# Performance work log

Measured on AMD Instinct MI355X. Metric: run time of the kernel, lower is better.

Reference implementation:

```python
import jax, jax.numpy as jnp
import numpy as np

GRID = (32, 32)          # 448 // 14
IMG = (448, 448)
SIGMA = 4.0              # anomalib AnomalyMapGenerator default smoothing


def _l2norm(x, axis=-1, eps=1e-12):
    return x / jnp.clip(jnp.linalg.norm(x, axis=axis, keepdims=True), eps, None)


def _gaussian_blur(x, sigma=SIGMA):
    # kornia-style: kernel_size = 2*int(4*sigma+0.5)+1, reflect padding, separable conv
    radius = int(4.0 * sigma + 0.5)
    t = jnp.arange(-radius, radius + 1, dtype=x.dtype)
    k = jnp.exp(-0.5 * (t / sigma) ** 2)
    k = k / k.sum()
    xp = jnp.pad(x, ((0, 0), (0, 0), (radius, radius), (radius, radius)), mode='reflect')
    kh = k.reshape(1, 1, -1, 1)
    kw = k.reshape(1, 1, 1, -1)
    dn = ('NCHW', 'OIHW', 'NCHW')
    y = jax.lax.conv_general_dilated(xp, kh, (1, 1), 'VALID', dimension_numbers=dn)
    return jax.lax.conv_general_dilated(y, kw, (1, 1), 'VALID', dimension_numbers=dn)


def setup_inputs() -> dict:
    key = jax.random.key(0)
    k1, k2 = jax.random.split(key)
    features = jax.random.normal(k1, (8, 1024, 384), dtype=jnp.float32)
    memory_bank = jax.random.normal(k2, (65536, 384), dtype=jnp.float32)
    return {"features": features, "memory_bank": memory_bank}


def reference(features, memory_bank):
    # features: (B, N, D) patch tokens from DINOv2; memory_bank: (M, D)
    b, n, _ = features.shape
    f = _l2norm(features)                 # F.normalize(features, p=2, dim=1) on flattened patches
    mb = _l2norm(memory_bank)             # bank stores normalized embeddings
    sim = jnp.einsum('bnd,md->bnm', f, mb)            # (B, N, M) cosine similarity
    dists = jnp.clip(1.0 - sim, 0.0, 2.0)
    min_dists = dists.min(axis=2)                     # k = num_neighbours = 1 -> row min
    num_top = max(int(n * 0.01), 1)
    top_vals = jax.lax.top_k(min_dists, num_top)[0]
    pred_score = top_vals.mean(axis=1, keepdims=True) # (B, 1)
    amap = min_dists.reshape(b, 1, *GRID)
    amap = jax.image.resize(amap, (b, 1, *IMG), method='bilinear')
    anomaly_map = _gaussian_blur(amap)                # (B, 1, H, W)
    return pred_score, anomaly_map
```

## Files before the change

kernel.cpp:

```cpp
#include <hip/hip_runtime.h>
#include <hip/hip_bf16.h>

#define NROW_F 8192
#define NROW_B 65536
#define KDIM   384
#define BM 128
#define BN 128
#define NSUB 16
#define NGRP (NROW_B / (BN * NSUB))
#define NBM  (NROW_F / BM)
#define NWG  (NBM * NGRP)

#define LDSA 0
#define LDSS2 0
#define LDSR2 16384
#define LDSB 49152
#define LDS_TOT 81920

typedef int   i32x4 __attribute__((ext_vector_type(4)));
typedef float f32x4 __attribute__((ext_vector_type(4)));

static __device__ __forceinline__ void stage16(const void* g, void* l) {
  __builtin_amdgcn_global_load_lds(
      (const __attribute__((address_space(1))) unsigned int*)g,
      (__attribute__((address_space(3))) unsigned int*)l, 16, 0, 0);
}

__global__ __launch_bounds__(256) void quantize_rows_kernel(
    const float* __restrict__ in, char* __restrict__ out8,
    float* __restrict__ scales, int nrows) {
  int row = blockIdx.x * 8 + (threadIdx.x >> 5);
  int l   = threadIdx.x & 31;
  if (row >= nrows) return;
  const f32x4* r = (const f32x4*)(in + (size_t)row * KDIM);
  f32x4 v[3];
  float ss = 0.f, mx = 0.f;
#pragma unroll
  for (int i = 0; i < 3; ++i) {
    v[i] = r[l + i * 32];
#pragma unroll
    for (int j = 0; j < 4; ++j) {
      ss += v[i][j] * v[i][j];
      mx = fmaxf(mx, fabsf(v[i][j]));
    }
  }
#pragma unroll
  for (int d = 1; d < 32; d <<= 1) {
    ss += __shfl_xor(ss, d, 64);
    mx = fmaxf(mx, __shfl_xor(mx, d, 64));
  }
  mx = fmaxf(mx, 1e-30f);
  float inv = rsqrtf(fmaxf(ss, 1e-24f));
  float scl = 127.0f / mx;
  if (l == 0) scales[row] = mx * inv * (1.0f / 127.0f);
  char* o = out8 + (size_t)row * KDIM;
#pragma unroll
  for (int i = 0; i < 3; ++i) {
    char4 c;
    c.x = (char)__float2int_rn(v[i][0] * scl);
    c.y = (char)__float2int_rn(v[i][1] * scl);
    c.z = (char)__float2int_rn(v[i][2] * scl);
    c.w = (char)__float2int_rn(v[i][3] * scl);
    *(char4*)(o + (l + i * 32) * 4) = c;
  }
}

__global__ __launch_bounds__(256, 2) void maxsim_kernel(
    const char* __restrict__ F8,
    const char* __restrict__ B8,
    const float* __restrict__ sA,
    const float* __restrict__ sB,
    float* __restrict__ partial) {
  __shared__ __align__(16) char smem[LDS_TOT];

  const int tid  = threadIdx.x;
  const int wv   = tid >> 6;
  const int lane = tid & 63;
  const int l15  = lane & 15;
  const int lhi  = lane >> 4;
  const int wr   = wv >> 1;
  const int wc   = wv & 1;

  const int wg  = (blockIdx.x & 7) * (NWG / 8) + (blockIdx.x >> 3);
  const int bm  = wg & (NBM - 1);
  const int grp = wg >> 6;
  const size_t brow = (size_t)bm * BM;

  const int srow = tid >> 2;
  const int gsw  = (tid & 3) ^ ((tid >> 3) & 3);

  {
    const char* gA = F8 + (size_t)(brow + srow) * KDIM + gsw * 16;
    char* lA = smem + LDSA + wv * 1024;
#pragma unroll
    for (int kt = 0; kt < 6; ++kt) {
      stage16(gA + kt * 64,             lA + kt * 8192);
      stage16(gA + kt * 64 + 64 * KDIM, lA + kt * 8192 + 4096);
    }
  }
  asm volatile("s_waitcnt vmcnt(0)" ::: "memory");
  __builtin_amdgcn_s_barrier();

  const int cof = ((l15 >> 1) & 3) << 4;
  auto ldA8 = [&](int k6, int m) -> i32x4 {
    int byte = k6 * 8192 + (wr * 64 + m * 16 + l15) * 64 + ((lhi << 4) ^ cof);
    return *reinterpret_cast<const i32x4*>(smem + LDSA + byte);
  };
  i32x4 a[6][4];
#pragma unroll
  for (int k6 = 0; k6 < 6; ++k6)
#pragma unroll
    for (int m = 0; m < 4; ++m) a[k6][m] = ldA8(k6, m);
  asm volatile("s_waitcnt lgkmcnt(0)" ::: "memory");
  __builtin_amdgcn_s_barrier();

  {
    const char* gs = (const char*)(sB + (size_t)grp * 2048) + tid * 16;
    stage16(gs,        smem + LDSS2 + wv * 1024);
    stage16(gs + 4096, smem + LDSS2 + 4096 + wv * 1024);
  }
  auto stageB = [&](int s2, int koff, int buf) {
    const char* g = B8 + ((size_t)grp * 2048 + s2 * 128 + srow) * KDIM
                    + koff * 64 + gsw * 16;
    char* l = smem + LDSB + buf * 8192 + wv * 1024;
    stage16(g, l);
    stage16(g + (size_t)64 * KDIM, l + 4096);
  };
  stageB(0, 0, 0);
  stageB(0, 1, 1);
  stageB(0, 2, 2);
  stageB(0, 3, 3);

  auto ldB8 = [&](int buf, int n) -> i32x4 {
    int byte = buf * 8192 + (wc * 64 + n * 16 + l15) * 64 + ((lhi << 4) ^ cof);
    return *reinterpret_cast<const i32x4*>(smem + LDSB + byte);
  };

  i32x4 acc[4][4];
  f32x4 vm[4];
#pragma unroll
  for (int m = 0; m < 4; ++m) {
    vm[m] = f32x4{-1e30f, -1e30f, -1e30f, -1e30f};
#pragma unroll
    for (int n = 0; n < 4; ++n) acc[m][n] = i32x4{0, 0, 0, 0};
  }

  asm volatile("s_waitcnt vmcnt(6)" ::: "memory");
  __builtin_amdgcn_s_barrier();

  i32x4 bA[4], bB[4];
#pragma unroll
  for (int n = 0; n < 4; ++n) bA[n] = ldB8(0, n);
  asm volatile("s_waitcnt lgkmcnt(0)" ::: "memory");

#define PHASE(K6, SUBX, RB, SBUF, BC, BN_) do {                               \
    asm volatile("s_waitcnt vmcnt(4)" ::: "memory");       \
    __builtin_amdgcn_s_barrier();                                             \
    __builtin_amdgcn_sched_barrier(0);                                        \
    _Pragma("unroll")                                                         \
    for (int n = 0; n < 4; ++n) BN_[n] = ldB8(RB, n);                         \
    stageB(((K6) < 2) ? (SUBX) : (((SUBX) + 1) & (NSUB - 1)),                 \
           ((K6) + 4) % 6, SBUF);                                             \
    __builtin_amdgcn_sched_barrier(0);                                        \
    __builtin_amdgcn_s_setprio(1);                                            \
    _Pragma("unroll")                                                         \
    for (int n = 0; n < 4; ++n)                                               \
      _Pragma("unroll")                                                       \
      for (int m = 0; m < 4; ++m)                                             \
        acc[m][n] = __builtin_amdgcn_mfma_i32_16x16x64_i8(                    \
            a[K6][m], BC[n], acc[m][n], 0, 0, 0);                             \
    __builtin_amdgcn_s_setprio(0);                                            \
    asm volatile("s_waitcnt lgkmcnt(0)" ::: "memory");                        \
    __builtin_amdgcn_sched_barrier(0);                                        \
  } while (0)

#define FOLD(S) do {                                                          \
    float sb[4];                                                              \
    _Pragma("unroll")                                                         \
    for (int n = 0; n < 4; ++n)                                               \
      sb[n] = *reinterpret_cast<const float*>(                                \
          smem + LDSS2 + ((S) * 128 + wc * 64 + n * 16 + l15) * 4);           \
    _Pragma("unroll")                                                         \
    for (int m = 0; m < 4; ++m) {                                             \
      _Pragma("unroll")                                                       \
      for (int n = 0; n < 4; ++n)                                             \
        _Pragma("unroll")                                                     \
        for (int j = 0; j < 4; ++j)                                           \
          vm[m][j] = fmaxf(vm[m][j], (float)acc[m][n][j] * sb[n]);            \
      _Pragma("unroll")                                                       \
      for (int n = 0; n < 4; ++n) acc[m][n] = i32x4{0, 0, 0, 0};              \
    }                                                                         \
  } while (0)

  for (int sub = 0; sub < NSUB; sub += 2) {
    PHASE(0, sub, 1, 0, bA, bB);
    PHASE(1, sub, 2, 1, bB, bA);
    PHASE(2, sub, 3, 2, bA, bB);
    PHASE(3, sub, 0, 3, bB, bA);
    PHASE(4, sub, 1, 0, bA, bB);
    PHASE(5, sub, 2, 1, bB, bA);
    FOLD(sub);
    PHASE(0, sub + 1, 3, 2, bA, bB);
    PHASE(1, sub + 1, 0, 3, bB, bA);
    PHASE(2, sub + 1, 1, 0, bA, bB);
    PHASE(3, sub + 1, 2, 1, bB, bA);
    PHASE(4, sub + 1, 3, 2, bA, bB);
    PHASE(5, sub + 1, 0, 3, bB, bA);
    FOLD(sub + 1);
  }
#undef PHASE
#undef FOLD

  asm volatile("s_waitcnt vmcnt(0)" ::: "memory");
#pragma unroll
  for (int d = 1; d < 16; d <<= 1)
#pragma unroll
    for (int m = 0; m < 4; ++m)
#pragma unroll
      for (int j = 0; j < 4; ++j)
        vm[m][j] = fmaxf(vm[m][j], __shfl_xor(vm[m][j], d, 64));

  float* red = (float*)(smem + LDSR2);
  __syncthreads();
  if (l15 == 0) {
#pragma unroll
    for (int m = 0; m < 4; ++m)
#pragma unroll
      for (int j = 0; j < 4; ++j)
        red[wc * 128 + wr * 64 + m * 16 + lhi * 4 + j] = vm[m][j];
  }
  __syncthreads();
  if (tid < BM) {
    float x = fmaxf(red[tid], red[128 + tid]);
    partial[(size_t)grp * NROW_F + brow + tid] = x * sA[brow + tid];
  }
}

__global__ __launch_bounds__(256) void combw_kernel(
    const float* __restrict__ partial, float* __restrict__ md,
    float* __restrict__ W) {
  if (blockIdx.x < 32) {
    int r = blockIdx.x * 256 + threadIdx.x;
    float m = -1e30f;
#pragma unroll
    for (int c = 0; c < NGRP; ++c) m = fmaxf(m, partial[(size_t)c * NROW_F + r]);
    float d = 1.0f - m;
    md[r] = fminf(fmaxf(d, 0.0f), 2.0f);
    return;
  }
  int idx = (blockIdx.x - 32) * 256 + threadIdx.x;
  int y = idx >> 5, g = idx & 31;
  float ksum = 0.f, acc = 0.f;
#pragma unroll
  for (int t = -16; t <= 16; ++t) {
    float ft = (float)t * 0.25f;
    float kv = expf(-0.5f * ft * ft);
    ksum += kv;
    int p = y + t;
    p = (p < 0) ? -p : ((p > 447) ? 894 - p : p);
    float src = ((float)p + 0.5f) * (1.0f / 14.0f) - 0.5f;
    float fl = floorf(src);
    int i0 = (int)fl;
    float fr = src - fl;
    int c0 = i0 < 0 ? 0 : (i0 > 31 ? 31 : i0);
    int i1 = i0 + 1;
    int c1 = i1 < 0 ? 0 : (i1 > 31 ? 31 : i1);
    float w = 0.f;
    if (c0 == g) w += 1.0f - fr;
    if (c1 == g) w += fr;
    acc += kv * w;
  }
  W[idx] = acc / ksum;
}

__global__ __launch_bounds__(64) void topk_kernel(
    const float* __restrict__ partial, float* __restrict__ out) {
  int b = blockIdx.x, lane = threadIdx.x;
  float vals[16];
#pragma unroll
  for (int k = 0; k < 16; ++k) {
    int r = b * 1024 + k * 64 + lane;
    float m = -1e30f;
#pragma unroll
    for (int c = 0; c < NGRP; ++c) m = fmaxf(m, partial[(size_t)c * NROW_F + r]);
    float d = 1.0f - m;
    vals[k] = fminf(fmaxf(d, 0.0f), 2.0f);
  }
  float total = 0.f;
  for (int it = 0; it < 10; ++it) {
    float lb = vals[0]; int li = 0;
#pragma unroll
    for (int k = 1; k < 16; ++k)
      if (vals[k] > lb) { lb = vals[k]; li = k; }
    float wm = lb;
#pragma unroll
    for (int d = 1; d < 64; d <<= 1) wm = fmaxf(wm, __shfl_xor(wm, d, 64));
    unsigned long long mask = __ballot(lb == wm);
    int winner = (int)(__ffsll(mask) - 1);
    bool kill = (lane == winner);
#pragma unroll
    for (int k = 0; k < 16; ++k)
      vals[k] = (kill && k == li) ? -1e30f : vals[k];
    total += wm;
  }
  if (lane == 0) out[b] = total * 0.1f;
}

__global__ __launch_bounds__(256) void map_kernel(
    const float* __restrict__ md, const float* __restrict__ W,
    float* __restrict__ out) {
  __shared__ float tmpv[32];
  int y = blockIdx.x % 448;
  int b = blockIdx.x / 448;
  int tid = threadIdx.x;
  if (tid < 32) {
    const float* w = W + y * 32;
    const float* m = md + b * 1024 + tid;
    float s = 0.f;
#pragma unroll
    for (int gy = 0; gy < 32; ++gy) s += w[gy] * m[gy * 32];
    tmpv[tid] = s;
  }
  __syncthreads();
  for (int x = tid; x < 448; x += 256) {
    const float* w = W + x * 32;
    float s = 0.f;
#pragma unroll
    for (int gx = 0; gx < 32; ++gx) s += w[gx] * tmpv[gx];
    out[(size_t)blockIdx.x * 448 + x] = s;
  }
}

extern "C" void kernel_launch(void* const* d_in, const int* in_sizes, int n_in,
                              void* d_out, int out_size, void* d_ws, size_t ws_size,
                              hipStream_t stream) {
  const float* features = (const float*)d_in[0];
  const float* bank     = (const float*)d_in[1];
  float* out = (float*)d_out;

  char* ws = (char*)d_ws;
  char*  mb8     = ws;
  char*  f8      = ws + 25165824;
  float* sB      = (float*)(ws + 28311552);
  float* sA      = (float*)(ws + 28573696);
  float* partial = (float*)(ws + 28606464);
  float* md      = (float*)(ws + 29655040);
  float* W       = (float*)(ws + 29687808);

  quantize_rows_kernel<<<NROW_B / 8, 256, 0, stream>>>(bank, mb8, sB, NROW_B);
  quantize_rows_kernel<<<NROW_F / 8, 256, 0, stream>>>(features, f8, sA, NROW_F);
  maxsim_kernel<<<NWG, 256, 0, stream>>>(f8, mb8, sA, sB, partial);
  combw_kernel<<<88, 256, 0, stream>>>(partial, md, W);
  topk_kernel<<<8, 64, 0, stream>>>(partial, out);
  map_kernel<<<8 * 448, 256, 0, stream>>>(md, W, out + 8);
}
```

Baseline: 239.6 us.

## Deepen B prefetch to six LDS buffers and process two k-chunks per barrier phase

The B-tile ring grows from four to six 8KB LDS slots. Two of the new slots reuse the A staging region, which is free once A has been copied into registers. Each pipeline phase now loads two k-chunks from LDS and runs 32 MFMAs before the next barrier, so there are half as many barrier/waitcnt phases per sub-tile. In exchange it uses more live B registers (four fragment sets instead of two) and a longer-lived prefetch that overlaps the reduction scratch area.

```diff
diff --git a/kernel.cpp b/kernel.cpp
--- a/kernel.cpp
+++ b/kernel.cpp
@@ -11,10 +11,9 @@
 #define NBM  (NROW_F / BM)
 #define NWG  (NBM * NGRP)
 
-#define LDSA 0
 #define LDSS2 0
 #define LDSR2 16384
-#define LDSB 49152
+#define BBASE(i) ((i) < 4 ? 49152 + 8192 * (i) : 24576 + 8192 * ((i) - 4))
 #define LDS_TOT 81920
 
 typedef int   i32x4 __attribute__((ext_vector_type(4)));
@@ -91,7 +90,7 @@
 
   {
     const char* gA = F8 + (size_t)(brow + srow) * KDIM + gsw * 16;
-    char* lA = smem + LDSA + wv * 1024;
+    char* lA = smem + wv * 1024;
 #pragma unroll
     for (int kt = 0; kt < 6; ++kt) {
       stage16(gA + kt * 64,             lA + kt * 8192);
@@ -104,7 +103,7 @@
   const int cof = ((l15 >> 1) & 3) << 4;
   auto ldA8 = [&](int k6, int m) -> i32x4 {
     int byte = k6 * 8192 + (wr * 64 + m * 16 + l15) * 64 + ((lhi << 4) ^ cof);
-    return *reinterpret_cast<const i32x4*>(smem + LDSA + byte);
+    return *reinterpret_cast<const i32x4*>(smem + byte);
   };
   i32x4 a[6][4];
 #pragma unroll
@@ -119,21 +118,25 @@
     stage16(gs,        smem + LDSS2 + wv * 1024);
     stage16(gs + 4096, smem + LDSS2 + 4096 + wv * 1024);
   }
-  auto stageB = [&](int s2, int koff, int buf) {
+  auto stageB = [&](int s2, int koff, int base) {
     const char* g = B8 + ((size_t)grp * 2048 + s2 * 128 + srow) * KDIM
                     + koff * 64 + gsw * 16;
-    char* l = smem + LDSB + buf * 8192 + wv * 1024;
+    char* l = smem + base + wv * 1024;
     stage16(g, l);
     stage16(g + (size_t)64 * KDIM, l + 4096);
   };
-  stageB(0, 0, 0);
-  stageB(0, 1, 1);
-  stageB(0, 2, 2);
-  stageB(0, 3, 3);
-
-  auto ldB8 = [&](int buf, int n) -> i32x4 {
-    int byte = buf * 8192 + (wc * 64 + n * 16 + l15) * 64 + ((lhi << 4) ^ cof);
-    return *reinterpret_cast<const i32x4*>(smem + LDSB + byte);
+#pragma unroll
+  for (int k = 0; k < 6; ++k) ;
+  stageB(0, 0, BBASE(0));
+  stageB(0, 1, BBASE(1));
+  stageB(0, 2, BBASE(2));
+  stageB(0, 3, BBASE(3));
+  stageB(0, 4, BBASE(4));
+  stageB(0, 5, BBASE(5));
+
+  auto ldB8 = [&](int base, int n) -> i32x4 {
+    int byte = base + (wc * 64 + n * 16 + l15) * 64 + ((lhi << 4) ^ cof);
+    return *reinterpret_cast<const i32x4*>(smem + byte);
   };
 
   i32x4 acc[4][4];
@@ -145,22 +148,26 @@
     for (int n = 0; n < 4; ++n) acc[m][n] = i32x4{0, 0, 0, 0};
   }
 
-  asm volatile("s_waitcnt vmcnt(6)" ::: "memory");
+  asm volatile("s_waitcnt vmcnt(8)" ::: "memory");
   __builtin_amdgcn_s_barrier();
 
-  i32x4 bA[4], bB[4];
-#pragma unroll
-  for (int n = 0; n < 4; ++n) bA[n] = ldB8(0, n);
+  i32x4 bP[4], bQ[4], bR[4], bS[4];
+#pragma unroll
+  for (int n = 0; n < 4; ++n) bP[n] = ldB8(BBASE(0), n);
+#pragma unroll
+  for (int n = 0; n < 4; ++n) bQ[n] = ldB8(BBASE(1), n);
   asm volatile("s_waitcnt lgkmcnt(0)" ::: "memory");
 
-#define PHASE(K6, SUBX, RB, SBUF, BC, BN_) do {                               \
-    asm volatile("s_waitcnt vmcnt(4)" ::: "memory");       \
+#define PHASE(PH, SUBX, CA, CB, NA, NB) do {                                  \
+    asm volatile("s_waitcnt vmcnt(4)" ::: "memory");                          \
     __builtin_amdgcn_s_barrier();                                             \
     __builtin_amdgcn_sched_barrier(0);                                        \
     _Pragma("unroll")                                                         \
-    for (int n = 0; n < 4; ++n) BN_[n] = ldB8(RB, n);                         \
-    stageB(((K6) < 2) ? (SUBX) : (((SUBX) + 1) & (NSUB - 1)),                 \
-           ((K6) + 4) % 6, SBUF);                                             \
+    for (int n = 0; n < 4; ++n) NA[n] = ldB8(BBASE((2 * (PH) + 2) % 6), n);   \
+    _Pragma("unroll")                                                         \
+    for (int n = 0; n < 4; ++n) NB[n] = ldB8(BBASE((2 * (PH) + 3) % 6), n);   \
+    stageB(((SUBX) + 1) & (NSUB - 1), 2 * (PH),     BBASE(2 * (PH)));         \
+    stageB(((SUBX) + 1) & (NSUB - 1), 2 * (PH) + 1, BBASE(2 * (PH) + 1));     \
     __builtin_amdgcn_sched_barrier(0);                                        \
     __builtin_amdgcn_s_setprio(1);                                            \
     _Pragma("unroll")                                                         \
@@ -168,7 +175,13 @@
       _Pragma("unroll")                                                       \
       for (int m = 0; m < 4; ++m)                                             \
         acc[m][n] = __builtin_amdgcn_mfma_i32_16x16x64_i8(                    \
-            a[K6][m], BC[n], acc[m][n], 0, 0, 0);                             \
+            a[2 * (PH)][m], CA[n], acc[m][n], 0, 0, 0);                       \
+    _Pragma("unroll")                                                         \
+    for (int n = 0; n < 4; ++n)                                               \
+      _Pragma("unroll")                                                       \
+      for (int m = 0; m < 4; ++m)                                             \
+        acc[m][n] = __builtin_amdgcn_mfma_i32_16x16x64_i8(                    \
+            a[2 * (PH) + 1][m], CB[n], acc[m][n], 0, 0, 0);                   \
     __builtin_amdgcn_s_setprio(0);                                            \
     asm volatile("s_waitcnt lgkmcnt(0)" ::: "memory");                        \
     __builtin_amdgcn_sched_barrier(0);                                        \
@@ -193,19 +206,13 @@
   } while (0)
 
   for (int sub = 0; sub < NSUB; sub += 2) {
-    PHASE(0, sub, 1, 0, bA, bB);
-    PHASE(1, sub, 2, 1, bB, bA);
-    PHASE(2, sub, 3, 2, bA, bB);
-    PHASE(3, sub, 0, 3, bB, bA);
-    PHASE(4, sub, 1, 0, bA, bB);
-    PHASE(5, sub, 2, 1, bB, bA);
+    PHASE(0, sub, bP, bQ, bR, bS);
+    PHASE(1, sub, bR, bS, bP, bQ);
+    PHASE(2, sub, bP, bQ, bR, bS);
     FOLD(sub);
-    PHASE(0, sub + 1, 3, 2, bA, bB);
-    PHASE(1, sub + 1, 0, 3, bB, bA);
-    PHASE(2, sub + 1, 1, 0, bA, bB);
-    PHASE(3, sub + 1, 2, 1, bB, bA);
-    PHASE(4, sub + 1, 3, 2, bA, bB);
-    PHASE(5, sub + 1, 0, 3, bB, bA);
+    PHASE(0, sub + 1, bR, bS, bP, bQ);
+    PHASE(1, sub + 1, bP, bQ, bR, bS);
+    PHASE(2, sub + 1, bR, bS, bP, bQ);
     FOLD(sub + 1);
   }
 #undef PHASE
```

Result: slower. 253.1 us (+5.6%).
